# Optimization experiments

Hardware: AMD Instinct MI355X
Metric: run time of the kernel (lower is better)

The kernel has to match this reference:

```python
import jax, jax.numpy as jnp
import numpy as np

D_MODEL = 2048
N_HEADS = 16
N_KV = 4
HEAD_DIM = 128
EPS = 1e-5


def _rmsnorm(x, w, eps=EPS):
    var = jnp.mean(x * x, axis=-1, keepdims=True)
    return x * jax.lax.rsqrt(var + eps) * w


def _rope_cos_sin(seq_len, head_dim, dtype):
    inv_freq = 1.0 / (10000.0 ** (jnp.arange(0, head_dim, 2, dtype=jnp.float32) / head_dim))
    t = jnp.arange(seq_len, dtype=jnp.float32)
    freqs = jnp.outer(t, inv_freq)  # [S, hd/2]
    return jnp.cos(freqs).astype(dtype), jnp.sin(freqs).astype(dtype)


def _apply_rope(x, cos, sin):
    # x: [B,H,S,hd]; cos/sin: [S,hd/2] broadcast as [1,1,S,hd/2]
    half = x.shape[-1] // 2
    x1, x2 = x[..., :half], x[..., half:]
    c = cos[None, None]
    s = sin[None, None]
    return jnp.concatenate([x1 * c - x2 * s, x1 * s + x2 * c], axis=-1)


def setup_inputs() -> dict:
    key = jax.random.key(0)
    ks = jax.random.split(key, 7)
    qkv_out = (N_HEADS + 2 * N_KV) * HEAD_DIM  # 3072
    d = D_MODEL
    inp = {
        "x": jax.random.normal(ks[0], (2, 2048, d), dtype=jnp.float32),
        "w_qkv": jax.random.normal(ks[1], (qkv_out, d), dtype=jnp.float32) * (1.0 / np.sqrt(d)),
        "q_norm_w": jnp.ones((HEAD_DIM,), dtype=jnp.float32),
        "k_norm_w": jnp.ones((HEAD_DIM,), dtype=jnp.float32),
        "w_gate": jax.random.normal(ks[2], (N_HEADS, d), dtype=jnp.float32) * 0.02,
        "b_gate": jnp.ones((N_HEADS,), dtype=jnp.float32),
        "w_o": jax.random.normal(ks[3], (d, N_HEADS * HEAD_DIM), dtype=jnp.float32) * (1.0 / np.sqrt(N_HEADS * HEAD_DIM)),
    }
    return inp


def reference(x, w_qkv, q_norm_w, k_norm_w, w_gate, b_gate, w_o):
    B, S, D = x.shape
    hd = HEAD_DIM
    scale = 1.0 / np.sqrt(hd)
    n_rep = N_HEADS // N_KV

    qkv = jnp.einsum("bsd,od->bso", x, w_qkv)  # [B,S,(H+2KV)*hd]
    q_size = N_HEADS * hd
    kv_size = N_KV * hd
    q = qkv[..., :q_size].reshape(B, S, N_HEADS, hd).transpose(0, 2, 1, 3)
    k = qkv[..., q_size:q_size + kv_size].reshape(B, S, N_KV, hd).transpose(0, 2, 1, 3)
    v = qkv[..., q_size + kv_size:].reshape(B, S, N_KV, hd).transpose(0, 2, 1, 3)

    q = _rmsnorm(q, q_norm_w)
    k = _rmsnorm(k, k_norm_w)

    cos, sin = _rope_cos_sin(S, hd, q.dtype)
    q = _apply_rope(q, cos, sin)
    k = _apply_rope(k, cos, sin)

    # GQA: repeat kv heads
    k = jnp.repeat(k, n_rep, axis=1)  # [B,H,S,hd]
    v = jnp.repeat(v, n_rep, axis=1)

    scores = jnp.einsum("bhqd,bhkd->bhqk", q, k) * scale
    causal = jnp.triu(jnp.ones((S, S), dtype=bool), k=1)
    neg = jnp.finfo(scores.dtype).min
    scores = jnp.where(causal[None, None], neg, scores)
    probs = jax.nn.softmax(scores, axis=-1)
    attn = jnp.einsum("bhqk,bhkd->bhqd", probs, v)  # [B,H,S,hd]

    # g1 gating on attention output per query head
    gate = jax.nn.sigmoid(jnp.einsum("bsd,hd->bsh", x, w_gate) + b_gate)  # [B,S,H]
    attn = attn * gate.transpose(0, 2, 1)[..., None]

    attn = attn.transpose(0, 2, 1, 3).reshape(B, S, N_HEADS * hd)
    out = jnp.einsum("bsf,df->bsd", attn, w_o)
    return out
```

## Files before the change

kernel.cpp:

```cpp
#include <hip/hip_runtime.h>

typedef __bf16 bf16x8 __attribute__((ext_vector_type(8)));
typedef float f32x4 __attribute__((ext_vector_type(4)));

typedef __attribute__((address_space(1))) void gvoid;
typedef __attribute__((address_space(3))) void lvoid;

__device__ __forceinline__ void gl_lds16(const void* g, void* l) {
    __builtin_amdgcn_global_load_lds((gvoid*)g, (lvoid*)l, 16, 0, 0);
}

__device__ __forceinline__ float fin(float v) {
    v = (v == v) ? v : 0.f;
    return fminf(fmaxf(v, -3.0e38f), 3.0e38f);
}

__device__ __forceinline__ bf16x8 cvt8(float4 a, float4 b) {
    bf16x8 r;
    r[0] = (__bf16)a.x; r[1] = (__bf16)a.y; r[2] = (__bf16)a.z; r[3] = (__bf16)a.w;
    r[4] = (__bf16)b.x; r[5] = (__bf16)b.y; r[6] = (__bf16)b.z; r[7] = (__bf16)b.w;
    return r;
}

__device__ __forceinline__ void cvt_range(const float* __restrict__ in,
                                          __bf16* __restrict__ out, int i) {
    const float4* p = (const float4*)in + (size_t)i * 2;
    ((bf16x8*)out)[i] = cvt8(p[0], p[1]);
}

__global__ __launch_bounds__(256) void prep_kernel(const float* __restrict__ x,
                                                   const float* __restrict__ wqkv,
                                                   __bf16* __restrict__ xb,
                                                   __bf16* __restrict__ wqb,
                                                   const float* __restrict__ wg,
                                                   const float* __restrict__ bg,
                                                   float* __restrict__ gate,
                                                   float2* __restrict__ ropet) {
    __shared__ float gp[4][16];
    int bid = blockIdx.x, tid = threadIdx.x;
    if (bid < 4096) {
        int lane = tid & 63, wave = tid >> 6;
        const float4* xr = (const float4*)(x + (size_t)bid * 2048);
        float4 p0 = xr[tid * 2], p1 = xr[tid * 2 + 1];
        ((bf16x8*)xb)[bid * 256 + tid] = cvt8(p0, p1);
#pragma unroll
        for (int h = 0; h < 16; ++h) {
            const float4* wr = (const float4*)(wg + (size_t)h * 2048);
            float4 w0 = wr[tid * 2], w1 = wr[tid * 2 + 1];
            float acc = p0.x * w0.x + p0.y * w0.y + p0.z * w0.z + p0.w * w0.w +
                        p1.x * w1.x + p1.y * w1.y + p1.z * w1.z + p1.w * w1.w;
#pragma unroll
            for (int m = 1; m < 64; m <<= 1) acc += __shfl_xor(acc, m);
            if (lane == 0) gp[wave][h] = acc;
        }
        __syncthreads();
        if (tid < 16) {
            int s = bid & 2047, b = bid >> 11;
            float z = gp[0][tid] + gp[1][tid] + gp[2][tid] + gp[3][tid] + bg[tid];
            gate[((size_t)b * 16 + tid) * 2048 + s] = 1.f / (1.f + __expf(-z));
        }
        return;
    }
    if (bid < 7168) {
        cvt_range(wqkv, wqb, (bid - 4096) * 256 + tid);
        return;
    }
    int idx = (bid - 7168) * 256 + tid;
    int s = idx >> 6, d0 = idx & 63;
    float freq = (float)s * __expf(-(float)d0 * (9.2103403719761836f / 64.0f));
    ropet[idx] = make_float2(cosf(freq), sinf(freq));
}

template <int WMT, int WNT, typename TC>
__global__ __launch_bounds__(512) void gemm8p(const __bf16* __restrict__ A,
                                              const __bf16* __restrict__ B,
                                              TC* __restrict__ C,
                                              int M, int N, int K) {
    constexpr int BM = WMT * 32;
    constexpr int BN = WNT * 64;
    constexpr int LA = BM / 128;
    constexpr int LB = BN / 128;
    constexpr int VMC = 2 * LA + LB;

    __shared__ __align__(16) __bf16 As[2][BM * 64];
    __shared__ __align__(16) __bf16 Bs[2][BN * 64];

    const int tid = threadIdx.x;
    const int lane = tid & 63, wave = tid >> 6;
    const int wm = wave >> 2, wn = wave & 3;
    const int quad = lane >> 4, mrow = lane & 15;

    const size_t row0 = (size_t)blockIdx.y * BM;
    const size_t col0 = (size_t)blockIdx.x * BN;

    size_t sA[LA], sB[LB];
    int dA[LA], dB[LB];
#pragma unroll
    for (int c = 0; c < LA; ++c) {
        int q = c * 512 + tid;
        int u = (q * 16) ^ ((((q * 16) >> 9) & 1) << 5);
        int rowl = ((u >> 10) >> 1) * 16 + ((u & 1023) >> 6);
        int col = ((u >> 10) & 1) * 32 + ((u & 63) >> 1);
        sA[c] = (size_t)rowl * K + col;
        dA[c] = q * 8;
    }
#pragma unroll
    for (int c = 0; c < LB; ++c) {
        int q = c * 512 + tid;
        int u = (q * 16) ^ ((((q * 16) >> 9) & 1) << 5);
        int rowl = ((u >> 10) >> 1) * 16 + ((u & 1023) >> 6);
        int col = ((u >> 10) & 1) * 32 + ((u & 63) >> 1);
        sB[c] = (size_t)rowl * K + col;
        dB[c] = q * 8;
    }

    const __bf16* Ag = A + row0 * K;
    const __bf16* Bg = B + col0 * K;

    f32x4 acc[WMT][WNT];
#pragma unroll
    for (int i = 0; i < WMT; ++i)
#pragma unroll
        for (int j = 0; j < WNT; ++j) acc[i][j] = (f32x4){0.f, 0.f, 0.f, 0.f};

    const int abase = (mrow * 64 + quad * 16) ^ ((mrow & 8) << 2);

    bf16x8 af[WMT / 2][2], bf[WNT / 2][2];

#define STA8(buf, h, kt)                                                        \
    _Pragma("unroll") for (int c = 0; c < LA; ++c)                              \
        gl_lds16(Ag + (size_t)(h) * (BM / 2) * K + (size_t)(kt) * 64 + sA[c],   \
                 &As[buf][(h) * (BM / 2) * 64 + dA[c]])

#define STB8(buf, h, kt)                                                        \
    _Pragma("unroll") for (int c = 0; c < LB; ++c)                              \
        gl_lds16(Bg + (size_t)(h) * (BN / 2) * K + (size_t)(kt) * 64 + sB[c],   \
                 &Bs[buf][(h) * (BN / 2) * 64 + dB[c]])

#define LDA8(buf, mh)                                                           \
    _Pragma("unroll") for (int m2 = 0; m2 < WMT / 2; ++m2)                      \
    _Pragma("unroll") for (int s = 0; s < 2; ++s)                               \
        af[m2][s] = *(const bf16x8*)((const char*)&As[buf][0] +                 \
            ((((mh) * (WMT / 2) + m2) * 2 + wm) * 2 + s) * 1024 + abase)

#define LDB8(buf, nh)                                                           \
    _Pragma("unroll") for (int n2 = 0; n2 < WNT / 2; ++n2)                      \
    _Pragma("unroll") for (int s = 0; s < 2; ++s)                               \
        bf[n2][s] = *(const bf16x8*)((const char*)&Bs[buf][0] +                 \
            ((((nh) * (WNT / 2) + n2) * 4 + wn) * 2 + s) * 1024 + abase)

#define MMA8(mh, nh)                                                            \
    _Pragma("unroll") for (int m2 = 0; m2 < WMT / 2; ++m2)                      \
    _Pragma("unroll") for (int n2 = 0; n2 < WNT / 2; ++n2)                      \
    _Pragma("unroll") for (int s = 0; s < 2; ++s)                               \
        acc[(mh) * (WMT / 2) + m2][(nh) * (WNT / 2) + n2] =                     \
            __builtin_amdgcn_mfma_f32_16x16x32_bf16(                            \
                af[m2][s], bf[n2][s],                                           \
                acc[(mh) * (WMT / 2) + m2][(nh) * (WNT / 2) + n2], 0, 0, 0)

#define BAR8 __builtin_amdgcn_s_barrier()

#define WAITVM                                                                  \
    do {                                                                        \
        if constexpr (VMC == 6)                                                 \
            asm volatile("s_waitcnt vmcnt(6)" ::: "memory");                    \
        else                                                                    \
            asm volatile("s_waitcnt vmcnt(4)" ::: "memory");                    \
    } while (0)

#define PHASE_TAIL(mh, nh)                                                      \
    __builtin_amdgcn_s_barrier();                                               \
    asm volatile("s_waitcnt lgkmcnt(0)" ::: "memory");                          \
    __builtin_amdgcn_sched_barrier(0);                                          \
    __builtin_amdgcn_s_setprio(1);                                              \
    MMA8(mh, nh);                                                               \
    __builtin_amdgcn_s_setprio(0)

    const int NT = K / 64;

    STA8(0, 0, 0);
    STB8(0, 0, 0);
    STA8(0, 1, 0);
    STB8(0, 1, 0);
    STA8(1, 0, 1);
    STB8(1, 1, 1);
    STA8(1, 1, 1);
    WAITVM;
    BAR8;

    for (int i = 0; i < NT / 2; ++i) {
        const int u = 2 * i;
        const int k2 = (u + 2 < NT) ? u + 2 : NT - 1;
        const int k3 = (u + 3 < NT) ? u + 3 : NT - 1;
        LDA8(0, 0); LDB8(0, 0); STB8(1, 0, u + 1);
        PHASE_TAIL(0, 0); BAR8;
        LDB8(0, 1); STA8(0, 0, k2);
        PHASE_TAIL(0, 1); BAR8;
        LDA8(0, 1); STB8(0, 1, k2);
        PHASE_TAIL(1, 1); BAR8;
        LDB8(0, 0); STA8(0, 1, k2);
        PHASE_TAIL(1, 0); WAITVM; BAR8;
        LDA8(1, 0); LDB8(1, 0); STB8(0, 0, k2);
        PHASE_TAIL(0, 0); BAR8;
        LDB8(1, 1); STA8(1, 0, k3);
        PHASE_TAIL(0, 1); BAR8;
        LDA8(1, 1); STB8(1, 1, k3);
        PHASE_TAIL(1, 1); BAR8;
        LDB8(1, 0); STA8(1, 1, k3);
        PHASE_TAIL(1, 0); WAITVM; BAR8;
    }
    asm volatile("s_waitcnt vmcnt(0)" ::: "memory");

#undef STA8
#undef STB8
#undef LDA8
#undef LDB8
#undef MMA8
#undef BAR8
#undef WAITVM
#undef PHASE_TAIL

#pragma unroll
    for (int mt = 0; mt < WMT; ++mt)
#pragma unroll
        for (int nt = 0; nt < WNT; ++nt)
#pragma unroll
            for (int r = 0; r < 4; ++r) {
                size_t row = row0 + (mt * 2 + wm) * 16 + quad * 4 + r;
                size_t col = col0 + (nt * 4 + wn) * 16 + mrow;
                C[row * N + col] = (TC)fin(acc[mt][nt][r]);
            }
}

#define SCALE_LOG2E 0.12751666797152713f

__global__ __launch_bounds__(256) void mid_kernel(const __bf16* __restrict__ qkv,
                                                  const float* __restrict__ qw,
                                                  const float* __restrict__ kw,
                                                  const float2* __restrict__ ropet,
                                                  __bf16* __restrict__ Q,
                                                  __bf16* __restrict__ Kx,
                                                  __bf16* __restrict__ Vt) {
    __shared__ __align__(16) __bf16 tile[64][72];
    int bid = blockIdx.x, t = threadIdx.x;
    if (bid < 20480) {
        int wid = bid * 4 + (t >> 6);
        int lane = t & 63;
        int head = wid % 20;
        int bs = wid / 20;
        int s = bs & 2047, b = bs >> 11;
        const __bf16* src;
        const float* w;
        __bf16* dst;
        float oscale;
        if (head < 16) {
            src = qkv + (size_t)bs * 3072 + head * 128;
            w = qw;
            dst = Q + ((size_t)(b * 16 + head) * 2048 + s) * 128;
            oscale = SCALE_LOG2E;
        } else {
            int kvh = head - 16;
            src = qkv + (size_t)bs * 3072 + 2048 + kvh * 128;
            w = kw;
            dst = Kx + ((size_t)(b * 4 + kvh) * 2048 + s) * 128;
            oscale = 1.0f;
        }
        float x1 = (float)src[lane], x2 = (float)src[lane + 64];
        float ss = x1 * x1 + x2 * x2;
#pragma unroll
        for (int m = 1; m < 64; m <<= 1) ss += __shfl_xor(ss, m);
        float inv = rsqrtf(ss * (1.0f / 128.0f) + 1e-5f);
        float y1 = x1 * inv * w[lane];
        float y2 = x2 * inv * w[lane + 64];
        float2 cs = ropet[s * 64 + lane];
        float c = cs.x, sn = cs.y;
        dst[lane] = (__bf16)((y1 * c - y2 * sn) * oscale);
        dst[lane + 64] = (__bf16)((y1 * sn + y2 * c) * oscale);
        return;
    }
    int v = bid - 20480;
    int st0 = (v & 31) * 64;
    int dblk = (v >> 5) & 1;
    int bz = v >> 6;
    int b = bz >> 2, kv = bz & 3;
    const __bf16* src = qkv + (size_t)(b * 2048 + st0) * 3072 + 2560 + kv * 128 + dblk * 64;
#pragma unroll
    for (int it = 0; it < 2; ++it) {
        int row = it * 32 + (t >> 3);
        int ch = t & 7;
        *(bf16x8*)&tile[row][ch * 8] = *(const bf16x8*)(src + (size_t)row * 3072 + ch * 8);
    }
    __syncthreads();
    __bf16* dst = Vt + ((size_t)(b * 4 + kv) * 128 + dblk * 64) * 2048 + st0;
#pragma unroll
    for (int it = 0; it < 2; ++it) {
        int drow = it * 32 + (t >> 3);
        int sch = t & 7;
        bf16x8 vv;
#pragma unroll
        for (int j = 0; j < 8; ++j) vv[j] = tile[sch * 8 + j][drow];
        *(bf16x8*)(dst + (size_t)drow * 2048 + sch * 8) = vv;
    }
}

#define FIXED_M 20.0f

#define MFMA16(a, b, c) __builtin_amdgcn_mfma_f32_16x16x32_bf16(a, b, c, 0, 0, 0)

template <int MODE>
__device__ __forceinline__ void attn_step(const __bf16* Kl, const __bf16* Vl,
                                          int ws, int quad, int mrow,
                                          const bf16x8* aq0, const bf16x8* aq1,
                                          f32x4* o0, f32x4* o1,
                                          float* l0, float* l1,
                                          __bf16* Pw) {
    f32x4 sc0[4], sc1[4];
    __builtin_amdgcn_s_setprio(1);
#pragma unroll
    for (int jt = 0; jt < 4; ++jt) {
        f32x4 s0 = (f32x4){0.f, 0.f, 0.f, 0.f};
        f32x4 s1 = (f32x4){0.f, 0.f, 0.f, 0.f};
#pragma unroll
        for (int dt = 0; dt < 4; ++dt) {
            bf16x8 bk = *(const bf16x8*)&Kl[((dt * 4 + quad) * 64 + jt * 16 + mrow) * 8];
            if (MODE < 2) s0 = MFMA16(aq0[dt], bk, s0);
            s1 = MFMA16(aq1[dt], bk, s1);
        }
        sc0[jt] = s0;
        sc1[jt] = s1;
    }
    __builtin_amdgcn_s_setprio(0);

    if (MODE == 1) {
        int rloc = ws * 16 + quad * 4;
#pragma unroll
        for (int jt = 0; jt < 4; ++jt)
#pragma unroll
            for (int r = 0; r < 4; ++r)
                if (jt * 16 + mrow > rloc + r) sc0[jt][r] = -1e30f;
    }
    if (MODE == 2) {
        int rloc = ws * 16 + quad * 4;
#pragma unroll
        for (int jt = 0; jt < 4; ++jt)
#pragma unroll
            for (int r = 0; r < 4; ++r)
                if (jt * 16 + mrow > rloc + r) sc1[jt][r] = -1e30f;
    }

    bf16x8 ap0[2], ap1[2];
    if (MODE < 2) {
#pragma unroll
        for (int r = 0; r < 4; ++r) {
            float ps = 0.f;
#pragma unroll
            for (int jt = 0; jt < 4; ++jt) {
                float pv = exp2f(sc0[jt][r] - FIXED_M);
                ps += pv;
                int k = jt * 16 + mrow;
                Pw[((k >> 3) * 16 + quad * 4 + r) * 8 + (k & 7)] = (__bf16)pv;
            }
#pragma unroll
            for (int off = 1; off < 16; off <<= 1) ps += __shfl_xor(ps, off);
            l0[r] += ps;
        }
#pragma unroll
        for (int ks = 0; ks < 2; ++ks)
            ap0[ks] = *(const bf16x8*)&Pw[((ks * 4 + quad) * 16 + mrow) * 8];
    }
#pragma unroll
    for (int r = 0; r < 4; ++r) {
        float ps = 0.f;
#pragma unroll
        for (int jt = 0; jt < 4; ++jt) {
            float pv = exp2f(sc1[jt][r] - FIXED_M);
            ps += pv;
            int k = jt * 16 + mrow;
            Pw[((k >> 3) * 16 + quad * 4 + r) * 8 + (k & 7)] = (__bf16)pv;
        }
#pragma unroll
        for (int off = 1; off < 16; off <<= 1) ps += __shfl_xor(ps, off);
        l1[r] += ps;
    }
#pragma unroll
    for (int ks = 0; ks < 2; ++ks)
        ap1[ks] = *(const bf16x8*)&Pw[((ks * 4 + quad) * 16 + mrow) * 8];

    __builtin_amdgcn_s_setprio(1);
#pragma unroll
    for (int d2 = 0; d2 < 8; ++d2)
#pragma unroll
        for (int ks = 0; ks < 2; ++ks) {
            bf16x8 bv = *(const bf16x8*)&Vl[((ks * 4 + quad) * 128 + d2 * 16 + mrow) * 8];
            if (MODE < 2) o0[d2] = MFMA16(ap0[ks], bv, o0[d2]);
            o1[d2] = MFMA16(ap1[ks], bv, o1[d2]);
        }
    __builtin_amdgcn_s_setprio(0);
}

__global__ __launch_bounds__(512, 2) void attn_kernel(const __bf16* __restrict__ Q,
                                                      const __bf16* __restrict__ Kx,
                                                      const __bf16* __restrict__ Vt,
                                                      const float* __restrict__ gate,
                                                      __bf16* __restrict__ O,
                                                      const float* __restrict__ wo,
                                                      __bf16* __restrict__ wob) {
    __shared__ __align__(16) __bf16 Kl[2][2][64 * 128];
    __shared__ __align__(16) __bf16 Vl[2][2][128 * 64];
    __shared__ __align__(16) __bf16 Pl[8][1024];
    int tid = threadIdx.x, lane = tid & 63, wave = tid >> 6;

    if (blockIdx.x >= 512) {
        cvt_range(wo, wob, ((int)blockIdx.x - 512) * 512 + tid);
        return;
    }

    int ws = wave & 3, st = wave >> 2;
    int quad = lane >> 4, mrow = lane & 15;
    __bf16* Pw = &Pl[wave][0];

    int idx = blockIdx.x;
    int qb = 15 - (idx >> 5);
    int h = idx & 15, b = (idx >> 4) & 1;
    int kvh = h >> 2;

    int sst = tid >> 8, lt = tid & 255;
    const __bf16* kbase = Kx + (size_t)(b * 4 + kvh) * 2048 * 128 + (lt & 63) * 128 + (lt >> 6) * 8;
    const __bf16* vbase = Vt + (size_t)(b * 4 + kvh) * 128 * 2048 + (lt & 127) * 2048 + (lt >> 7) * 8;
    int ldst = lt * 8;

    auto STAGE = [&](int buf, int tile) {
        const __bf16* kp = kbase + (size_t)tile * 8192;
        const __bf16* vp = vbase + (size_t)tile * 64;
#pragma unroll
        for (int c = 0; c < 4; ++c) gl_lds16(kp + 32 * c, &Kl[sst][buf][ldst + 2048 * c]);
#pragma unroll
        for (int c = 0; c < 4; ++c) gl_lds16(vp + 16 * c, &Vl[sst][buf][ldst + 2048 * c]);
    };

    STAGE(0, sst);

    const __bf16* Qh = Q + ((size_t)(b * 16 + h) * 2048 + qb * 128 + ws * 16 + mrow) * 128;
    bf16x8 aq0[4], aq1[4];
#pragma unroll
    for (int dt = 0; dt < 4; ++dt) {
        aq0[dt] = *(const bf16x8*)(Qh + dt * 32 + quad * 8);
        aq1[dt] = *(const bf16x8*)(Qh + 8192 + dt * 32 + quad * 8);
    }

    f32x4 o0[8], o1[8];
#pragma unroll
    for (int d2 = 0; d2 < 8; ++d2) {
        o0[d2] = (f32x4){0.f, 0.f, 0.f, 0.f};
        o1[d2] = (f32x4){0.f, 0.f, 0.f, 0.f};
    }
    float l0[4] = {0.f, 0.f, 0.f, 0.f}, l1[4] = {0.f, 0.f, 0.f, 0.f};

    __syncthreads();

    int cur = 0;
    for (int kt = 0; kt < qb; ++kt) {
        STAGE(cur ^ 1, 2 * (kt + 1) + sst);
        attn_step<0>(Kl[st][cur], Vl[st][cur], ws, quad, mrow, aq0, aq1, o0, o1, l0, l1, Pw);
        __syncthreads();
        cur ^= 1;
    }
    if (st == 0)
        attn_step<1>(Kl[0][cur], Vl[0][cur], ws, quad, mrow, aq0, aq1, o0, o1, l0, l1, Pw);
    else
        attn_step<2>(Kl[1][cur], Vl[1][cur], ws, quad, mrow, aq0, aq1, o0, o1, l0, l1, Pw);

    __syncthreads();
    f32x4* mo = (f32x4*)&Kl[0][0][0];
    float* ml = (float*)&Pl[0][0];
    int mlane = ws * 64 + lane;
    if (st == 1) {
#pragma unroll
        for (int d2 = 0; d2 < 8; ++d2) {
            mo[d2 * 256 + mlane] = o0[d2];
            mo[(d2 + 8) * 256 + mlane] = o1[d2];
        }
#pragma unroll
        for (int r = 0; r < 4; ++r) {
            ml[r * 256 + mlane] = l0[r];
            ml[(r + 4) * 256 + mlane] = l1[r];
        }
    }
    __syncthreads();
    if (st == 0) {
#pragma unroll
        for (int d2 = 0; d2 < 8; ++d2) {
            o0[d2] += mo[d2 * 256 + mlane];
            o1[d2] += mo[(d2 + 8) * 256 + mlane];
        }
#pragma unroll
        for (int r = 0; r < 4; ++r) {
            l0[r] += ml[r * 256 + mlane];
            l1[r] += ml[(r + 4) * 256 + mlane];
        }
#pragma unroll
        for (int hf = 0; hf < 2; ++hf) {
            f32x4* oo = hf ? o1 : o0;
            float* ll = hf ? l1 : l0;
            int srow0 = qb * 128 + hf * 64 + ws * 16 + quad * 4;
            float gv[4], il[4];
#pragma unroll
            for (int r = 0; r < 4; ++r) {
                gv[r] = gate[((size_t)b * 16 + h) * 2048 + srow0 + r];
                il[r] = 1.0f / fmaxf(ll[r], 1e-30f);
            }
#pragma unroll
            for (int d2 = 0; d2 < 8; ++d2)
#pragma unroll
                for (int r = 0; r < 4; ++r)
                    O[(size_t)(b * 2048 + srow0 + r) * 2048 + h * 128 + d2 * 16 + mrow] =
                        (__bf16)fin(oo[d2][r] * il[r] * gv[r]);
        }
    }
}

extern "C" void kernel_launch(void* const* d_in, const int* in_sizes, int n_in,
                              void* d_out, int out_size, void* d_ws, size_t ws_size,
                              hipStream_t stream) {
    const float* x = (const float*)d_in[0];
    const float* w_qkv = (const float*)d_in[1];
    const float* q_norm_w = (const float*)d_in[2];
    const float* k_norm_w = (const float*)d_in[3];
    const float* w_gate = (const float*)d_in[4];
    const float* b_gate = (const float*)d_in[5];
    const float* w_o = (const float*)d_in[6];
    float* out = (float*)d_out;

    char* ws = (char*)d_ws;
    char* od = (char*)d_out;
    __bf16* xb = (__bf16*)(od);
    __bf16* wqb = (__bf16*)(od + 16777216);
    float* gateb = (float*)(od + 29360128);
    float2* ropet = (float2*)(od + 29622272);
    __bf16* Qb = (__bf16*)(od);
    __bf16* qkv = (__bf16*)(ws);
    __bf16* attnb = (__bf16*)(ws);
    __bf16* wob = (__bf16*)(ws + 16777216);
    __bf16* Kb = (__bf16*)(ws + 25165824);
    __bf16* Vtb = (__bf16*)(ws + 29360128);

    prep_kernel<<<7680, 256, 0, stream>>>(x, w_qkv, xb, wqb, w_gate, b_gate, gateb, ropet);
    gemm8p<8, 4, __bf16><<<dim3(3072 / 256, 4096 / 256), 512, 0, stream>>>(
        xb, wqb, qkv, 4096, 3072, 2048);
    mid_kernel<<<20992, 256, 0, stream>>>(qkv, q_norm_w, k_norm_w, ropet, Qb, Kb, Vtb);
    attn_kernel<<<1536, 512, 0, stream>>>(Qb, Kb, Vtb, gateb, attnb, w_o, wob);
    gemm8p<4, 4, float><<<dim3(2048 / 256, 4096 / 128), 512, 0, stream>>>(
        attnb, wob, out, 4096, 2048, 2048);
}
```

Before: 359.1 us.

## Fuse K RMSNorm and RoPE into QKV GEMM epilogue, remap workgroup order

The QKV GEMM epilogue now applies RMSNorm and RoPE directly to the K-head column blocks. It computes row sums of squares through shuffles plus an LDS reduction and writes K in its final layout, so the mid kernel only handles Q heads and the V transpose. The GEMM also remaps workgroup IDs in an XCD-aware interleaved order, meant to improve L2 locality across the chiplets. This saves a qkv round trip for K and some launch work, at the cost of extra epilogue work and divergence in two column blocks.

Result: no change. 358.6 us (-0.1%).

```diff
diff --git a/kernel.cpp b/kernel.cpp
--- a/kernel.cpp
+++ b/kernel.cpp
@@ -71,11 +71,14 @@
     ropet[idx] = make_float2(cosf(freq), sinf(freq));
 }
 
-template <int WMT, int WNT, typename TC>
+template <int WMT, int WNT, int EPI, typename TC>
 __global__ __launch_bounds__(512) void gemm8p(const __bf16* __restrict__ A,
                                               const __bf16* __restrict__ B,
                                               TC* __restrict__ C,
-                                              int M, int N, int K) {
+                                              int M, int N, int K,
+                                              const float* __restrict__ kw,
+                                              const float2* __restrict__ ropet,
+                                              __bf16* __restrict__ Kx) {
     constexpr int BM = WMT * 32;
     constexpr int BN = WNT * 64;
     constexpr int LA = BM / 128;
@@ -90,8 +93,12 @@
     const int wm = wave >> 2, wn = wave & 3;
     const int quad = lane >> 4, mrow = lane & 15;
 
-    const size_t row0 = (size_t)blockIdx.y * BM;
-    const size_t col0 = (size_t)blockIdx.x * BN;
+    const int nbx = gridDim.x;
+    const int nwg = nbx * gridDim.y;
+    const int orig = (int)blockIdx.y * nbx + (int)blockIdx.x;
+    const int wg = (orig & 7) * (nwg >> 3) + (orig >> 3);
+    const size_t row0 = (size_t)(wg / nbx) * BM;
+    const size_t col0 = (size_t)(wg % nbx) * BN;
 
     size_t sA[LA], sB[LB];
     int dA[LA], dB[LB];
@@ -220,6 +227,60 @@
 #undef WAITVM
 #undef PHASE_TAIL
 
+    if constexpr (EPI) {
+        int xblk = (int)(col0 >> 8);
+        if (xblk == 8 || xblk == 9) {
+            __syncthreads();
+            float* sums = (float*)&As[0][0];
+            const int d0 = wn * 16 + mrow;
+#pragma unroll
+            for (int mt = 0; mt < WMT; ++mt)
+#pragma unroll
+                for (int t = 0; t < 2; ++t) {
+                    f32x4 p;
+#pragma unroll
+                    for (int r = 0; r < 4; ++r)
+                        p[r] = acc[mt][2 * t][r] * acc[mt][2 * t][r] +
+                               acc[mt][2 * t + 1][r] * acc[mt][2 * t + 1][r];
+#pragma unroll
+                    for (int m = 1; m < 16; m <<= 1)
+#pragma unroll
+                        for (int r = 0; r < 4; ++r) p[r] += __shfl_xor(p[r], m);
+                    if (mrow == 0) {
+                        int idx = ((((wm * 8 + mt) * 4 + quad) * 2 + t) * 4 + wn) * 4;
+#pragma unroll
+                        for (int r = 0; r < 4; ++r) sums[idx + r] = p[r];
+                    }
+                }
+            __syncthreads();
+            float w1 = kw[d0], w2 = kw[d0 + 64];
+#pragma unroll
+            for (int mt = 0; mt < WMT; ++mt) {
+                int rbase = (int)row0 + (mt * 2 + wm) * 16 + quad * 4;
+#pragma unroll
+                for (int t = 0; t < 2; ++t) {
+                    int ib = (((wm * 8 + mt) * 4 + quad) * 2 + t) * 16;
+                    f32x4 sv = *(const f32x4*)&sums[ib] + *(const f32x4*)&sums[ib + 4] +
+                               *(const f32x4*)&sums[ib + 8] + *(const f32x4*)&sums[ib + 12];
+                    int kvh = (xblk - 8) * 2 + t;
+#pragma unroll
+                    for (int r = 0; r < 4; ++r) {
+                        int row = rbase + r;
+                        int s_ = row & 2047, b_ = row >> 11;
+                        float inv = rsqrtf(sv[r] * (1.0f / 128.0f) + 1e-5f);
+                        float2 cs = ropet[s_ * 64 + d0];
+                        float y1 = acc[mt][2 * t][r] * inv * w1;
+                        float y2 = acc[mt][2 * t + 1][r] * inv * w2;
+                        __bf16* dst = Kx + (((size_t)(b_ * 4 + kvh) * 2048 + s_) << 7);
+                        dst[d0] = (__bf16)(y1 * cs.x - y2 * cs.y);
+                        dst[d0 + 64] = (__bf16)(y1 * cs.y + y2 * cs.x);
+                    }
+                }
+            }
+            return;
+        }
+    }
+
 #pragma unroll
     for (int mt = 0; mt < WMT; ++mt)
 #pragma unroll
@@ -236,49 +297,32 @@
 
 __global__ __launch_bounds__(256) void mid_kernel(const __bf16* __restrict__ qkv,
                                                   const float* __restrict__ qw,
-                                                  const float* __restrict__ kw,
                                                   const float2* __restrict__ ropet,
                                                   __bf16* __restrict__ Q,
-                                                  __bf16* __restrict__ Kx,
                                                   __bf16* __restrict__ Vt) {
     __shared__ __align__(16) __bf16 tile[64][72];
     int bid = blockIdx.x, t = threadIdx.x;
-    if (bid < 20480) {
+    if (bid < 16384) {
         int wid = bid * 4 + (t >> 6);
         int lane = t & 63;
-        int head = wid % 20;
-        int bs = wid / 20;
+        int head = wid & 15;
+        int bs = wid >> 4;
         int s = bs & 2047, b = bs >> 11;
-        const __bf16* src;
-        const float* w;
-        __bf16* dst;
-        float oscale;
-        if (head < 16) {
-            src = qkv + (size_t)bs * 3072 + head * 128;
-            w = qw;
-            dst = Q + ((size_t)(b * 16 + head) * 2048 + s) * 128;
-            oscale = SCALE_LOG2E;
-        } else {
-            int kvh = head - 16;
-            src = qkv + (size_t)bs * 3072 + 2048 + kvh * 128;
-            w = kw;
-            dst = Kx + ((size_t)(b * 4 + kvh) * 2048 + s) * 128;
-            oscale = 1.0f;
-        }
+        const __bf16* src = qkv + (size_t)bs * 3072 + head * 128;
+        __bf16* dst = Q + ((size_t)(b * 16 + head) * 2048 + s) * 128;
         float x1 = (float)src[lane], x2 = (float)src[lane + 64];
         float ss = x1 * x1 + x2 * x2;
 #pragma unroll
         for (int m = 1; m < 64; m <<= 1) ss += __shfl_xor(ss, m);
         float inv = rsqrtf(ss * (1.0f / 128.0f) + 1e-5f);
-        float y1 = x1 * inv * w[lane];
-        float y2 = x2 * inv * w[lane + 64];
+        float y1 = x1 * inv * qw[lane];
+        float y2 = x2 * inv * qw[lane + 64];
         float2 cs = ropet[s * 64 + lane];
-        float c = cs.x, sn = cs.y;
-        dst[lane] = (__bf16)((y1 * c - y2 * sn) * oscale);
-        dst[lane + 64] = (__bf16)((y1 * sn + y2 * c) * oscale);
+        dst[lane] = (__bf16)((y1 * cs.x - y2 * cs.y) * SCALE_LOG2E);
+        dst[lane + 64] = (__bf16)((y1 * cs.y + y2 * cs.x) * SCALE_LOG2E);
         return;
     }
-    int v = bid - 20480;
+    int v = bid - 16384;
     int st0 = (v & 31) * 64;
     int dblk = (v >> 5) & 1;
     int bz = v >> 6;
@@ -545,10 +589,10 @@
     __bf16* Vtb = (__bf16*)(ws + 29360128);
 
     prep_kernel<<<7680, 256, 0, stream>>>(x, w_qkv, xb, wqb, w_gate, b_gate, gateb, ropet);
-    gemm8p<8, 4, __bf16><<<dim3(3072 / 256, 4096 / 256), 512, 0, stream>>>(
-        xb, wqb, qkv, 4096, 3072, 2048);
-    mid_kernel<<<20992, 256, 0, stream>>>(qkv, q_norm_w, k_norm_w, ropet, Qb, Kb, Vtb);
+    gemm8p<8, 4, 1, __bf16><<<dim3(3072 / 256, 4096 / 256), 512, 0, stream>>>(
+        xb, wqb, qkv, 4096, 3072, 2048, k_norm_w, ropet, Kb);
+    mid_kernel<<<16896, 256, 0, stream>>>(qkv, q_norm_w, ropet, Qb, Vtb);
     attn_kernel<<<1536, 512, 0, stream>>>(Qb, Kb, Vtb, gateb, attnb, w_o, wob);
-    gemm8p<4, 4, float><<<dim3(2048 / 256, 4096 / 128), 512, 0, stream>>>(
-        attnb, wob, out, 4096, 2048, 2048);
-}
+    gemm8p<4, 4, 0, float><<<dim3(2048 / 256, 4096 / 128), 512, 0, stream>>>(
+        attnb, wob, out, 4096, 2048, 2048, nullptr, nullptr, nullptr);
+}
```
